# Performance work log

Hardware: AMD Instinct MI355X
Metric: run time of the kernel (lower is better)

The kernel has to match this reference:

```python
import jax, jax.numpy as jnp
import numpy as np

N_NODES = 100000
N_CAND = 32768
HIDDEN = 1024
N_REL = 10


def setup_inputs() -> dict:
    key = jax.random.key(0)
    k0, k1, k2, k3, k4, k5 = jax.random.split(key, 6)
    node_embeddings = jax.random.normal(k0, (N_NODES, HIDDEN), dtype=jnp.float32)
    src_idx = jax.random.randint(k1, (N_CAND,), 0, N_NODES, dtype=jnp.int32)
    dst_idx = jax.random.randint(k2, (N_CAND,), 0, N_NODES, dtype=jnp.int32)
    labels = jax.random.randint(k3, (N_CAND,), 0, N_REL, dtype=jnp.int32)
    # Linear weights stored as [in, out] so forward is x @ W + b
    W1 = jax.random.normal(k4, (4 * HIDDEN, HIDDEN), dtype=jnp.float32) * (1.0 / np.sqrt(4 * HIDDEN))
    b1 = jnp.zeros((HIDDEN,), dtype=jnp.float32)
    W2 = jax.random.normal(k5, (HIDDEN, N_REL), dtype=jnp.float32) * (1.0 / np.sqrt(HIDDEN))
    b2 = jnp.zeros((N_REL,), dtype=jnp.float32)
    return {"node_embeddings": node_embeddings, "src_idx": src_idx, "dst_idx": dst_idx,
            "labels": labels, "W1": W1, "b1": b1, "W2": W2, "b2": b2}


def reference(node_embeddings, src_idx, dst_idx, labels, W1, b1, W2, b2):
    # Vectorized gather of candidate endpoints (replaces Python loop)
    src = node_embeddings[src_idx]            # [C, H]
    dst = node_embeddings[dst_idx]            # [C, H]
    feats = jnp.concatenate([src, dst, jnp.abs(src - dst), src * dst], axis=-1)  # [C, 4H]
    h = jax.nn.gelu(feats @ W1 + b1, approximate=False)  # exact GELU, matches torch default
    # Dropout is identity in eval mode
    logits = h @ W2 + b2                      # [C, n_rel]
    logp = jax.nn.log_softmax(logits, axis=-1)
    loss = -jnp.mean(jnp.take_along_axis(logp, labels[:, None].astype(jnp.int32), axis=-1))
    return loss, logits
```

## Files before the change

kernel.cpp:

```cpp
#include <hip/hip_runtime.h>
#include <stdint.h>

#define CANDS 32768
#define HID   1024
#define KDIM  4096
#define NREL  10

typedef __attribute__((ext_vector_type(8))) short bf16x8;
typedef __attribute__((ext_vector_type(4))) float f32x4;

__device__ __forceinline__ float bf2f(unsigned short u) {
  union { unsigned int i; float f; } v; v.i = ((unsigned int)u) << 16; return v.f;
}
__device__ __forceinline__ unsigned short f2bf(float f) {
  union { float f; unsigned int i; } v; v.f = f;
  unsigned int x = v.i;
  return (unsigned short)((x + 0x7FFFu + ((x >> 16) & 1u)) >> 16);
}
__device__ __forceinline__ void async16(const void* g, void* l) {
  __builtin_amdgcn_global_load_lds(
      (const __attribute__((address_space(1))) unsigned int*)(uintptr_t)g,
      (__attribute__((address_space(3))) unsigned int*)(uintptr_t)l,
      16, 0, 0);
}

__global__ void transpose_w1(const float* __restrict__ W1,
                             unsigned short* __restrict__ W1T) {
  __shared__ __align__(16) unsigned short tile[64][72];
  int bk = blockIdx.x;
  int bn = blockIdx.y;
  int t = threadIdx.x;
  int r = t >> 3, c8 = (t & 7) * 8;
  for (int i = 0; i < 2; ++i) {
    int rr = r + i * 32;
    const float4* src = (const float4*)(W1 + (size_t)(bk * 64 + rr) * HID + bn * 64 + c8);
    float4 v0 = src[0], v1 = src[1];
    tile[rr][c8 + 0] = f2bf(v0.x); tile[rr][c8 + 1] = f2bf(v0.y);
    tile[rr][c8 + 2] = f2bf(v0.z); tile[rr][c8 + 3] = f2bf(v0.w);
    tile[rr][c8 + 4] = f2bf(v1.x); tile[rr][c8 + 5] = f2bf(v1.y);
    tile[rr][c8 + 6] = f2bf(v1.z); tile[rr][c8 + 7] = f2bf(v1.w);
  }
  __syncthreads();
  for (int i = 0; i < 2; ++i) {
    int rr = r + i * 32;
    unsigned short tmp[8];
    for (int j = 0; j < 8; ++j) tmp[j] = tile[c8 + j][rr];
    ushort4* dst = (ushort4*)(W1T + (size_t)(bn * 64 + rr) * KDIM + bk * 64 + c8);
    dst[0] = *(ushort4*)&tmp[0];
    dst[1] = *(ushort4*)&tmp[4];
  }
}

__global__ __launch_bounds__(256) void build_feats(
    const float* __restrict__ emb,
    const int* __restrict__ sidx,
    const int* __restrict__ didx,
    unsigned short* __restrict__ feats) {
  int t = threadIdx.x;
  for (int m = blockIdx.x; m < CANDS; m += gridDim.x) {
    const float* srow = emb + (size_t)sidx[m] * HID;
    const float* drow = emb + (size_t)didx[m] * HID;
    float4 s4 = *(const float4*)(srow + t * 4);
    float4 d4 = *(const float4*)(drow + t * 4);
    unsigned short* o = feats + (size_t)m * KDIM;
    ushort4 sv, dv, av, pv;
    sv.x = f2bf(s4.x); sv.y = f2bf(s4.y); sv.z = f2bf(s4.z); sv.w = f2bf(s4.w);
    dv.x = f2bf(d4.x); dv.y = f2bf(d4.y); dv.z = f2bf(d4.z); dv.w = f2bf(d4.w);
    av.x = f2bf(fabsf(s4.x - d4.x)); av.y = f2bf(fabsf(s4.y - d4.y));
    av.z = f2bf(fabsf(s4.z - d4.z)); av.w = f2bf(fabsf(s4.w - d4.w));
    pv.x = f2bf(s4.x * d4.x); pv.y = f2bf(s4.y * d4.y);
    pv.z = f2bf(s4.z * d4.z); pv.w = f2bf(s4.w * d4.w);
    *(ushort4*)(o + t * 4)           = sv;
    *(ushort4*)(o + HID + t * 4)     = dv;
    *(ushort4*)(o + 2 * HID + t * 4) = av;
    *(ushort4*)(o + 3 * HID + t * 4) = pv;
  }
}

#define G1_BM 256
#define G1_BN 256
#define G1_BK 64
#define G1_NT (KDIM / G1_BK)

__global__ __launch_bounds__(512, 2) void gemm1_gelu(
    const unsigned short* __restrict__ A,
    const unsigned short* __restrict__ BT,
    const float* __restrict__ b1,
    unsigned short* __restrict__ H) {
  extern __shared__ __align__(16) unsigned short smem[];

  int bid = blockIdx.x;
  int wg  = (bid & 7) * 64 + (bid >> 3);
  int m0 = (wg >> 2) * G1_BM;
  int n0 = (wg & 3) * G1_BN;

  int t = threadIdx.x;
  int lane = t & 63, w = t >> 6;
  int wm = w >> 2, wn = w & 3;
  int quad = lane >> 4, l16 = lane & 15;

  int tr = t >> 3;
  int slot = t & 7;
  int gk8 = (slot ^ (tr & 7)) * 8;
  const unsigned short* gA = A  + (size_t)(m0 + tr) * KDIM + gk8;
  const unsigned short* gB = BT + (size_t)(n0 + tr) * KDIM + gk8;
  int lidx = t * 8;

  int sx = l16 & 7;
  int aoff = (wm * 128 + l16) * G1_BK + ((quad ^ sx) * 8);
  int boff = (wn * 64  + l16) * G1_BK + ((quad ^ sx) * 8);

  f32x4 acc[8][4] = {};

#define G1_STAGE(b, kkelem) do {                                               \
    unsigned short* la_ = smem + (b) * 32768;                                  \
    unsigned short* lb_ = la_ + 16384;                                         \
    _Pragma("unroll")                                                          \
    for (int l_ = 0; l_ < 4; ++l_)                                             \
      async16(gA + (size_t)l_ * 64 * KDIM + (kkelem), la_ + l_ * 4096 + lidx); \
    _Pragma("unroll")                                                          \
    for (int l_ = 0; l_ < 4; ++l_)                                             \
      async16(gB + (size_t)l_ * 64 * KDIM + (kkelem), lb_ + l_ * 4096 + lidx); \
  } while (0)

  G1_STAGE(0, 0);
  for (int kt = 0; kt < G1_NT; ++kt) {
    int c = kt & 1;
    if (kt + 1 < G1_NT) {
      G1_STAGE(c ^ 1, (kt + 1) * G1_BK);
      asm volatile("s_waitcnt vmcnt(8)" ::: "memory");
    } else {
      asm volatile("s_waitcnt vmcnt(0)" ::: "memory");
    }
    __builtin_amdgcn_s_barrier();
    asm volatile("" ::: "memory");
    const unsigned short* bufA = smem + c * 32768;
    const unsigned short* bufB = bufA + 16384;
    __builtin_amdgcn_s_setprio(1);
#pragma unroll
    for (int h = 0; h < 2; ++h) {
      bf16x8 bfr[4], afr[8];
#pragma unroll
      for (int j = 0; j < 4; ++j)
        bfr[j] = *(const bf16x8*)&bufB[(boff ^ (h << 5)) + j * 1024];
#pragma unroll
      for (int i = 0; i < 8; ++i)
        afr[i] = *(const bf16x8*)&bufA[(aoff ^ (h << 5)) + i * 1024];
#pragma unroll
      for (int i = 0; i < 8; ++i)
#pragma unroll
        for (int j = 0; j < 4; ++j)
          acc[i][j] = __builtin_amdgcn_mfma_f32_16x16x32_bf16(afr[i], bfr[j], acc[i][j], 0, 0, 0);
    }
    __builtin_amdgcn_s_setprio(0);
    asm volatile("" ::: "memory");
    __builtin_amdgcn_s_barrier();
  }

#pragma unroll
  for (int j = 0; j < 4; ++j) {
    int n = n0 + wn * 64 + j * 16 + l16;
    float bias = b1[n];
#pragma unroll
    for (int i = 0; i < 8; ++i) {
#pragma unroll
      for (int r = 0; r < 4; ++r) {
        int m = m0 + wm * 128 + i * 16 + quad * 4 + r;
        float x = acc[i][j][r] + bias;
        float g = 0.5f * x * (1.0f + erff(x * 0.70710678118654752f));
        H[(size_t)m * HID + n] = f2bf(g);
      }
    }
  }
#undef G1_STAGE
}

__global__ __launch_bounds__(256) void gemm2_loss(
    const unsigned short* __restrict__ H,
    const float* __restrict__ W2,
    const float* __restrict__ b2,
    const int* __restrict__ labels,
    float* __restrict__ out,
    float* __restrict__ gacc) {
#define W2P 1032
  __shared__ __align__(16) unsigned short w2t[16 * W2P];
  __shared__ float lacc;
  int t = threadIdx.x;
  int lane = t & 63, wave = t >> 6;
  int quad = lane >> 4, l16 = lane & 15;
  if (t == 0) lacc = 0.0f;
  for (int k = t; k < HID; k += 256) {
    for (int j = 0; j < NREL; ++j) w2t[j * W2P + k] = f2bf(W2[(size_t)k * NREL + j]);
    for (int j = NREL; j < 16; ++j) w2t[j * W2P + k] = 0;
  }
  __syncthreads();

  int r0 = blockIdx.x * 64 + wave * 16;
  const unsigned short* hrow = H + (size_t)(r0 + l16) * HID;
  f32x4 acc = {};
#pragma unroll 8
  for (int s = 0; s < 32; ++s) {
    bf16x8 a = *(const bf16x8*)(hrow + s * 32 + quad * 8);
    bf16x8 b = *(const bf16x8*)&w2t[l16 * W2P + s * 32 + quad * 8];
    acc = __builtin_amdgcn_mfma_f32_16x16x32_bf16(a, b, acc, 0, 0, 0);
  }

  int col = l16;
  float bias = (col < NREL) ? b2[col] : 0.0f;
  float local = 0.0f;
#pragma unroll
  for (int r = 0; r < 4; ++r) {
    int row = r0 + quad * 4 + r;
    float x = acc[r] + bias;
    float v = (col < NREL) ? x : -1e30f;
    float mx = v;
    for (int d = 1; d < 16; d <<= 1) mx = fmaxf(mx, __shfl_xor(mx, d));
    float e = (col < NREL) ? expf(x - mx) : 0.0f;
    float se = e;
    for (int d = 1; d < 16; d <<= 1) se += __shfl_xor(se, d);
    float lse = mx + logf(se);
    if (col < NREL) {
      out[1 + (size_t)row * NREL + col] = x;
      if (labels[row] == col) local += (lse - x);
    }
  }
  atomicAdd(&lacc, local);
  __syncthreads();
  if (t == 0) atomicAdd(gacc, lacc);
}

__global__ void finalize_loss(const float* __restrict__ gacc, float* __restrict__ out) {
  out[0] = *gacc * (1.0f / (float)CANDS);
}

extern "C" void kernel_launch(void* const* d_in, const int* in_sizes, int n_in,
                              void* d_out, int out_size, void* d_ws, size_t ws_size,
                              hipStream_t stream) {
  const float* emb    = (const float*)d_in[0];
  const int*   sidx   = (const int*)d_in[1];
  const int*   didx   = (const int*)d_in[2];
  const int*   labels = (const int*)d_in[3];
  const float* W1     = (const float*)d_in[4];
  const float* b1     = (const float*)d_in[5];
  const float* W2     = (const float*)d_in[6];
  const float* b2     = (const float*)d_in[7];
  float* out = (float*)d_out;

  char* ws = (char*)d_ws;
  float*          gacc  = (float*)ws;
  unsigned short* W1T   = (unsigned short*)(ws + 256);
  unsigned short* feats = (unsigned short*)(ws + 256 + 8388608);
  unsigned short* H     = (unsigned short*)(ws + 256 + 8388608 + 268435456);

  static bool g1_attr_set = false;
  if (!g1_attr_set) {
    (void)hipFuncSetAttribute((const void*)gemm1_gelu,
                              hipFuncAttributeMaxDynamicSharedMemorySize, 131072);
    g1_attr_set = true;
  }

  hipMemsetAsync(gacc, 0, sizeof(float), stream);
  transpose_w1<<<dim3(64, 16), 256, 0, stream>>>(W1, W1T);
  build_feats<<<2048, 256, 0, stream>>>(emb, sidx, didx, feats);
  gemm1_gelu<<<512, 512, 131072, stream>>>(feats, W1T, b1, H);
  gemm2_loss<<<CANDS / 64, 256, 0, stream>>>(H, W2, b2, labels, out, gacc);
  finalize_loss<<<1, 1, 0, stream>>>(gacc, out);
}
```

Baseline: 876.5 us.

## Split GEMM1 k-tile into four phases interleaving LDS reads, prefetch and MFMA

Restructures the GEMM1 main loop into an 8-phase ping-pong schedule. Each k-tile is split into four phases, and each phase reads a slice of A fragments from LDS, issues part of the next tile's global-to-LDS loads for A or B, and runs its MFMAs between barriers. The intent is finer-grained overlap of global loads, LDS reads and matrix math, plus lower register pressure from holding only two A fragments at a time. In exchange there are many more barriers per tile and fragile vmcnt accounting.

After: 819.7 us. -6.5%, faster.

```diff
diff --git a/kernel.cpp b/kernel.cpp
--- a/kernel.cpp
+++ b/kernel.cpp
@@ -110,51 +110,79 @@
   int aoff = (wm * 128 + l16) * G1_BK + ((quad ^ sx) * 8);
   int boff = (wn * 64  + l16) * G1_BK + ((quad ^ sx) * 8);
 
+  unsigned short* bufA0 = smem;
+  unsigned short* bufB0 = smem + 16384;
+  unsigned short* bufA1 = smem + 32768;
+  unsigned short* bufB1 = smem + 49152;
+
   f32x4 acc[8][4] = {};
-
-#define G1_STAGE(b, kkelem) do {                                               \
-    unsigned short* la_ = smem + (b) * 32768;                                  \
-    unsigned short* lb_ = la_ + 16384;                                         \
-    _Pragma("unroll")                                                          \
-    for (int l_ = 0; l_ < 4; ++l_)                                             \
-      async16(gA + (size_t)l_ * 64 * KDIM + (kkelem), la_ + l_ * 4096 + lidx); \
-    _Pragma("unroll")                                                          \
-    for (int l_ = 0; l_ < 4; ++l_)                                             \
-      async16(gB + (size_t)l_ * 64 * KDIM + (kkelem), lb_ + l_ * 4096 + lidx); \
+  bf16x8 bfr[4][2];
+  bf16x8 af[2][2];
+
+#define STG_A(DST, ktile) do { _Pragma("unroll")                                 \
+    for (int l_ = 0; l_ < 4; ++l_)                                               \
+      async16(gA + (size_t)l_ * 64 * KDIM + (ktile) * G1_BK,                     \
+              (DST) + l_ * 4096 + lidx); } while (0)
+#define STG_BLO(DST, ktile) do { _Pragma("unroll")                               \
+    for (int l_ = 0; l_ < 2; ++l_)                                               \
+      async16(gB + (size_t)l_ * 64 * KDIM + (ktile) * G1_BK,                     \
+              (DST) + l_ * 4096 + lidx); } while (0)
+#define STG_BHI(DST, ktile) do { _Pragma("unroll")                               \
+    for (int l_ = 2; l_ < 4; ++l_)                                               \
+      async16(gB + (size_t)l_ * 64 * KDIM + (ktile) * G1_BK,                     \
+              (DST) + l_ * 4096 + lidx); } while (0)
+
+#define PHASE(qq, AB, BB, LOADB, TAILWAIT, ...) do {                             \
+    if (LOADB) {                                                                 \
+      _Pragma("unroll") for (int j_ = 0; j_ < 4; ++j_)                           \
+        _Pragma("unroll") for (int h_ = 0; h_ < 2; ++h_)                         \
+          bfr[j_][h_] = *(const bf16x8*)&(BB)[(boff ^ (h_ << 5)) + j_ * 1024];   \
+    }                                                                            \
+    _Pragma("unroll") for (int i_ = 0; i_ < 2; ++i_)                             \
+      _Pragma("unroll") for (int h_ = 0; h_ < 2; ++h_)                           \
+        af[i_][h_] = *(const bf16x8*)&(AB)[(aoff ^ (h_ << 5)) + (2*(qq)+i_) * 1024]; \
+    __VA_ARGS__;                                                                 \
+    asm volatile("" ::: "memory");                                               \
+    __builtin_amdgcn_s_barrier();                                                \
+    asm volatile("s_waitcnt lgkmcnt(0)" ::: "memory");                           \
+    __builtin_amdgcn_sched_barrier(0);                                           \
+    __builtin_amdgcn_s_setprio(1);                                               \
+    _Pragma("unroll") for (int h_ = 0; h_ < 2; ++h_)                             \
+      _Pragma("unroll") for (int i_ = 0; i_ < 2; ++i_)                           \
+        _Pragma("unroll") for (int j_ = 0; j_ < 4; ++j_)                         \
+          acc[2*(qq)+i_][j_] = __builtin_amdgcn_mfma_f32_16x16x32_bf16(          \
+              af[i_][h_], bfr[j_][h_], acc[2*(qq)+i_][j_], 0, 0, 0);             \
+    __builtin_amdgcn_s_setprio(0);                                               \
+    TAILWAIT;                                                                    \
+    asm volatile("" ::: "memory");                                               \
+    __builtin_amdgcn_s_barrier();                                                \
+    asm volatile("" ::: "memory");                                               \
   } while (0)
 
-  G1_STAGE(0, 0);
-  for (int kt = 0; kt < G1_NT; ++kt) {
-    int c = kt & 1;
-    if (kt + 1 < G1_NT) {
-      G1_STAGE(c ^ 1, (kt + 1) * G1_BK);
-      asm volatile("s_waitcnt vmcnt(8)" ::: "memory");
-    } else {
-      asm volatile("s_waitcnt vmcnt(0)" ::: "memory");
-    }
-    __builtin_amdgcn_s_barrier();
-    asm volatile("" ::: "memory");
-    const unsigned short* bufA = smem + c * 32768;
-    const unsigned short* bufB = bufA + 16384;
-    __builtin_amdgcn_s_setprio(1);
-#pragma unroll
-    for (int h = 0; h < 2; ++h) {
-      bf16x8 bfr[4], afr[8];
-#pragma unroll
-      for (int j = 0; j < 4; ++j)
-        bfr[j] = *(const bf16x8*)&bufB[(boff ^ (h << 5)) + j * 1024];
-#pragma unroll
-      for (int i = 0; i < 8; ++i)
-        afr[i] = *(const bf16x8*)&bufA[(aoff ^ (h << 5)) + i * 1024];
-#pragma unroll
-      for (int i = 0; i < 8; ++i)
-#pragma unroll
-        for (int j = 0; j < 4; ++j)
-          acc[i][j] = __builtin_amdgcn_mfma_f32_16x16x32_bf16(afr[i], bfr[j], acc[i][j], 0, 0, 0);
-    }
-    __builtin_amdgcn_s_setprio(0);
-    asm volatile("" ::: "memory");
-    __builtin_amdgcn_s_barrier();
+#define W_PH3 do { if (kt + 2 < G1_NT)                                           \
+      asm volatile("s_waitcnt vmcnt(4)" ::: "memory");                           \
+    else asm volatile("s_waitcnt vmcnt(0)" ::: "memory"); } while (0)
+#define W_PH7 do { if (kt + 2 < G1_NT)                                           \
+      asm volatile("s_waitcnt vmcnt(4)" ::: "memory"); } while (0)
+#define W_NONE do {} while (0)
+
+  STG_A(bufA0, 0);
+  STG_BLO(bufB0, 0); STG_BHI(bufB0, 0);
+  STG_BLO(bufB1, 1); STG_BHI(bufB1, 1);
+  asm volatile("s_waitcnt vmcnt(4)" ::: "memory");
+  asm volatile("" ::: "memory");
+  __builtin_amdgcn_s_barrier();
+  asm volatile("" ::: "memory");
+
+  for (int kt = 0; kt < G1_NT; kt += 2) {
+    PHASE(0, bufA0, bufB0, 1, W_NONE, STG_A(bufA1, kt + 1));
+    PHASE(1, bufA0, bufB0, 0, W_NONE, if (kt + 2 < G1_NT) STG_BLO(bufB0, kt + 2));
+    PHASE(2, bufA0, bufB0, 0, W_NONE, if (kt + 2 < G1_NT) STG_BHI(bufB0, kt + 2));
+    PHASE(3, bufA0, bufB0, 0, W_PH3, );
+    PHASE(0, bufA1, bufB1, 1, W_NONE, if (kt + 2 < G1_NT) STG_A(bufA0, kt + 2));
+    PHASE(1, bufA1, bufB1, 0, W_NONE, if (kt + 3 < G1_NT) STG_BLO(bufB1, kt + 3));
+    PHASE(2, bufA1, bufB1, 0, W_NONE, if (kt + 3 < G1_NT) STG_BHI(bufB1, kt + 3));
+    PHASE(3, bufA1, bufB1, 0, W_PH7, );
   }
 
 #pragma unroll
@@ -172,7 +200,13 @@
       }
     }
   }
-#undef G1_STAGE
+#undef STG_A
+#undef STG_BLO
+#undef STG_BHI
+#undef PHASE
+#undef W_PH3
+#undef W_PH7
+#undef W_NONE
 }
 
 __global__ __launch_bounds__(256) void gemm2_loss(
```
